# Kernel tuning notes

Hardware: AMD Instinct MI355X
Metric: run time of the kernel (lower is better)

The kernel has to match this reference:

```python
import jax, jax.numpy as jnp
import numpy as np

B, S, H, D, P = 16, 512, 12, 768, 256
TOP_RATE = 0.1
K = int(round(TOP_RATE * S))  # 51, matches round(self.top_rate * hidden_state.size(1))
LN_EPS = 1e-5


def setup_inputs() -> dict:
    key = jax.random.key(0)
    ks = jax.random.split(key, 6)
    return {
        "hidden_state": jax.random.normal(ks[0], (B, S, D), dtype=jnp.float32),
        "attention": jax.random.normal(ks[1], (B, H, S, S), dtype=jnp.float32),
        "length": S,  # uniform valid length (scalar int)
        # node_trans: Linear(D, P)
        "W_node": jax.random.normal(ks[2], (D, P), dtype=jnp.float32) * 0.02,
        "b_node": jnp.zeros((P,), dtype=jnp.float32),
        # node_eta parameter, initialized to 0 (self.node_eta.data.fill_(0))
        "node_eta": jnp.zeros((1,), dtype=jnp.float32),
        # fc: Linear(P, P)
        "W_fc": jax.random.normal(ks[3], (P, P), dtype=jnp.float32) * 0.02,
        "b_fc": jnp.zeros((P,), dtype=jnp.float32),
        # LayerNorm(P)
        "ln_gamma": jnp.ones((P,), dtype=jnp.float32),
        "ln_beta": jnp.zeros((P,), dtype=jnp.float32),
    }


def reference(hidden_state, attention, W_node, b_node, node_eta, W_fc, b_fc,
              ln_gamma, ln_beta, length):
    # average attention over heads: [B, S, S]
    avg_atten = attention.mean(axis=1)
    # per-target-node top-k neighbors
    vals, idx = jax.lax.top_k(avg_atten, K)  # [B, S, K]
    # edge mask replicating softmax(where(v>0, v, -1e9)) followed by nonzero():
    # entries at -1e9 underflow to exactly 0 in fp32 softmax iff the row has a
    # positive value; otherwise the softmax is uniform and all edges survive.
    keep = vals > 0.0
    row_has_pos = keep.any(axis=-1, keepdims=True)
    keep = jnp.where(row_has_pos, keep, True)            # [B, S, K] (>=1 True per row)
    keepf = keep.astype(hidden_state.dtype)[..., None]   # [B, S, K, 1]

    # node_trans on all nodes: [B, S, P]
    h = hidden_state @ W_node + b_node

    # gather source-node features h[b, idx[b, t, j], :] -> [B, S, K, P]
    gathered = jax.vmap(lambda hb, ib: hb[ib])(h, idx)

    # reduce='mean': edge weight w=1, mailbox mean over kept incoming edges
    h_agg = (gathered * keepf).sum(axis=2) / keepf.sum(axis=2)

    eta = node_eta[0]
    new_h = eta * h + (1.0 - eta) * h_agg                # [B, S, P]

    # dgl.mean_nodes: mean over the `length` nodes of each sub-graph (=S here)
    out = new_h.mean(axis=1)                             # [B, P]

    # fc(dropout(tanh(out))) with dropout in eval mode (identity)
    out = jnp.tanh(out) @ W_fc + b_fc

    # LayerNorm
    mu = out.mean(axis=-1, keepdims=True)
    var = ((out - mu) ** 2).mean(axis=-1, keepdims=True)
    out = (out - mu) / jnp.sqrt(var + LN_EPS) * ln_gamma + ln_beta
    return out
```

## Files before the change

### kernel.cpp

```cpp
#include <hip/hip_runtime.h>
#include <math.h>

#define B_ 16
#define S_ 512
#define H_ 12
#define D_ 768
#define P_ 256
#define K_ 51
#define CH_ 16
#define NCHUNK_ (S_/CH_)

__device__ __forceinline__ unsigned okey(float f) {
  unsigned u = __float_as_uint(f);
  return (u & 0x80000000u) ? ~u : (u | 0x80000000u);
}

__global__ __launch_bounds__(256, 8) void k1_topk_mask(
    const float* __restrict__ attn, unsigned long long* __restrict__ maskbuf,
    float* __restrict__ invbuf) {
  const int tid = threadIdx.x;
  const int wv = tid >> 6;
  const int lane = tid & 63;
  const int bt = blockIdx.x * 4 + wv;
  const int b = bt >> 9;
  const int t = bt & (S_ - 1);

  const float* base = attn + (((size_t)b * H_) * S_ + t) * S_;
  float a[8] = {0.f, 0.f, 0.f, 0.f, 0.f, 0.f, 0.f, 0.f};
  #pragma unroll
  for (int h = 0; h < H_; ++h) {
    const float* r = base + (size_t)h * (S_ * S_);
    const float4 u = *(const float4*)(r + 4 * lane);
    const float4 v = *(const float4*)(r + 256 + 4 * lane);
    a[0] += u.x; a[1] += u.y; a[2] += u.z; a[3] += u.w;
    a[4] += v.x; a[5] += v.y; a[6] += v.z; a[7] += v.w;
  }
  unsigned k[8];
  #pragma unroll
  for (int i = 0; i < 8; ++i) {
    a[i] *= (1.0f / (float)H_);
    k[i] = okey(a[i]);
  }

  int p = 0;
  #pragma unroll
  for (int i = 0; i < 8; ++i) p += __popcll(__ballot(a[i] > 0.f));

  bool sel[8];
  float invcnt;
  if (p >= 1 && p < K_) {
    #pragma unroll
    for (int i = 0; i < 8; ++i) sel[i] = (a[i] > 0.f);
    invcnt = 1.0f / (float)p;
  } else {
    unsigned prefix = 0;
    unsigned rem = K_;
    #pragma unroll
    for (int bpos = 31; bpos >= 0; --bpos) {
      const unsigned cand = prefix | (1u << bpos);
      const unsigned ch = cand >> bpos;
      unsigned cnt = 0;
      #pragma unroll
      for (int i = 0; i < 8; ++i)
        cnt += (unsigned)__popcll(__ballot((k[i] >> bpos) == ch));
      const bool ge = (cnt >= rem);
      prefix = ge ? cand : prefix;
      rem = ge ? rem : (rem - cnt);
    }
    const unsigned T = prefix;
    unsigned long long mm[8];
    #pragma unroll
    for (int i = 0; i < 8; ++i) mm[i] = __ballot(k[i] == T);
    const unsigned long long lt = ((unsigned long long)1 << lane) - 1ull;
    int fh = 0;
    #pragma unroll
    for (int i = 0; i < 4; ++i) fh += __popcll(mm[i]);
    #pragma unroll
    for (int i = 0; i < 8; ++i) {
      sel[i] = (k[i] > T);
      if (k[i] == T) {
        int r = 0;
        if (i < 4) {
          #pragma unroll
          for (int i2 = 0; i2 < 4; ++i2) r += __popcll(mm[i2] & lt);
          for (int i2 = 0; i2 < i; ++i2) r += (int)((mm[i2] >> lane) & 1ull);
        } else {
          r = fh;
          #pragma unroll
          for (int i2 = 4; i2 < 8; ++i2) r += __popcll(mm[i2] & lt);
          for (int i2 = 4; i2 < i; ++i2) r += (int)((mm[i2] >> lane) & 1ull);
        }
        if (r < (int)rem) sel[i] = true;
      }
    }
    invcnt = 1.0f / (float)K_;
  }

  unsigned long long m[8];
  #pragma unroll
  for (int i = 0; i < 8; ++i) m[i] = __ballot(sel[i]);
  if (lane == 0) {
    ulonglong2* mp = (ulonglong2*)(maskbuf + (size_t)bt * 8);
    mp[0] = ulonglong2{m[0], m[1]};
    mp[1] = ulonglong2{m[2], m[3]};
    mp[2] = ulonglong2{m[4], m[5]};
    mp[3] = ulonglong2{m[6], m[7]};
    invbuf[bt] = invcnt;
  }
}

__global__ __launch_bounds__(192) void k2_colsum_wsum(
    const unsigned long long* __restrict__ maskbuf,
    const float* __restrict__ invbuf, const float* __restrict__ node_eta,
    const float* __restrict__ hidden, float* __restrict__ x_part) {
  const int chunk = blockIdx.x;
  const int b = blockIdx.y;
  const int tid = threadIdx.x;
  __shared__ unsigned long long ld[S_ * 4];
  __shared__ float inv[S_];
  __shared__ float part[16][8];
  __shared__ float cs[CH_];

  const int wi0 = (chunk < 16) ? 0 : 4;
  for (int i = tid; i < S_ * 4; i += 192) {
    const int t = i >> 2, j = i & 3;
    ld[i] = maskbuf[(((size_t)b << 9) + t) * 8 + wi0 + j];
  }
  for (int i = tid; i < S_; i += 192) inv[i] = invbuf[(b << 9) + i];
  __syncthreads();

  if (tid < 128) {
    const int c = tid >> 3, g = tid & 7;
    const int s = chunk * CH_ + c;
    const int j = s & 3;
    const unsigned long long bm = 1ull << ((s & 255) >> 2);
    float w = 0.f;
    #pragma unroll 8
    for (int i = 0; i < 64; ++i) {
      const int t = i * 8 + g;
      if (ld[t * 4 + j] & bm) w += inv[t];
    }
    part[c][g] = w;
  }
  __syncthreads();
  if (tid < CH_) {
    float w = 0.f;
    #pragma unroll
    for (int g = 0; g < 8; ++g) w += part[tid][g];
    const float eta = node_eta[0];
    cs[tid] = (eta + (1.0f - eta) * w) * (1.0f / (float)S_);
  }
  __syncthreads();

  const float* hb = hidden + ((size_t)b * S_ + (size_t)chunk * CH_) * D_ + 4 * tid;
  float4 acc = make_float4(0.f, 0.f, 0.f, 0.f);
  #pragma unroll
  for (int s = 0; s < CH_; ++s) {
    const float4 v = *(const float4*)(hb + (size_t)s * D_);
    const float c = cs[s];
    acc.x += c * v.x; acc.y += c * v.y; acc.z += c * v.z; acc.w += c * v.w;
  }
  *(float4*)(x_part + ((size_t)chunk * B_ + b) * D_ + 4 * tid) = acc;
}

__global__ __launch_bounds__(256) void k3_tail(
    const float* __restrict__ x_part, const float* __restrict__ W_node,
    const float* __restrict__ b_node, const float* __restrict__ W_fc,
    const float* __restrict__ b_fc, const float* __restrict__ gamma,
    const float* __restrict__ beta, float* __restrict__ out) {
  const int b = blockIdx.x;
  const int tid = threadIdx.x;
  __shared__ float xs[D_];
  __shared__ float ts[P_];
  __shared__ float red[4];

  #pragma unroll
  for (int d = tid; d < D_; d += 256) {
    float s = 0.f;
    #pragma unroll 8
    for (int c = 0; c < NCHUNK_; ++c)
      s += x_part[((size_t)c * B_ + b) * D_ + d];
    xs[d] = s;
  }
  __syncthreads();

  float acc = 0.f;
  #pragma unroll 8
  for (int d = 0; d < D_; ++d) acc += xs[d] * W_node[(size_t)d * P_ + tid];
  ts[tid] = tanhf(acc + b_node[tid]);
  __syncthreads();

  float o = 0.f;
  #pragma unroll 8
  for (int q = 0; q < P_; ++q) o += ts[q] * W_fc[(size_t)q * P_ + tid];
  o += b_fc[tid];

  float s = o;
  #pragma unroll
  for (int off = 32; off > 0; off >>= 1) s += __shfl_down(s, off, 64);
  const int wave = tid >> 6, lane = tid & 63;
  if (lane == 0) red[wave] = s;
  __syncthreads();
  const float mu = (red[0] + red[1] + red[2] + red[3]) * (1.0f / (float)P_);
  __syncthreads();
  const float dv = o - mu;
  float s2 = dv * dv;
  #pragma unroll
  for (int off = 32; off > 0; off >>= 1) s2 += __shfl_down(s2, off, 64);
  if (lane == 0) red[wave] = s2;
  __syncthreads();
  const float var = (red[0] + red[1] + red[2] + red[3]) * (1.0f / (float)P_);
  const float inv = 1.0f / sqrtf(var + 1e-5f);
  out[b * P_ + tid] = dv * inv * gamma[tid] + beta[tid];
}

extern "C" void kernel_launch(void* const* d_in, const int* in_sizes, int n_in,
                              void* d_out, int out_size, void* d_ws, size_t ws_size,
                              hipStream_t stream) {
  (void)in_sizes; (void)n_in; (void)out_size; (void)ws_size;
  const float* hidden   = (const float*)d_in[0];
  const float* attn     = (const float*)d_in[1];
  const float* W_node   = (const float*)d_in[3];
  const float* b_node   = (const float*)d_in[4];
  const float* node_eta = (const float*)d_in[5];
  const float* W_fc     = (const float*)d_in[6];
  const float* b_fc     = (const float*)d_in[7];
  const float* gamma    = (const float*)d_in[8];
  const float* beta     = (const float*)d_in[9];
  float* out = (float*)d_out;

  unsigned long long* maskbuf = (unsigned long long*)d_ws;
  float* invbuf = (float*)(maskbuf + (size_t)B_ * S_ * 8);
  float* x_part = invbuf + B_ * S_;

  k1_topk_mask<<<(B_ * S_) / 4, 256, 0, stream>>>(attn, maskbuf, invbuf);
  k2_colsum_wsum<<<dim3(NCHUNK_, B_), 192, 0, stream>>>(maskbuf, invbuf,
                                                        node_eta, hidden, x_part);
  k3_tail<<<B_, 256, 0, stream>>>(x_part, W_node, b_node, W_fc, b_fc,
                                  gamma, beta, out);
}
```

Measured before the change: 383.2 us.

## Split serial tail kernel into parallel reduce, matvec, fc and layernorm kernels

The single 16-block tail kernel, which did the chunk reduction, both matvecs and the layernorm serially per batch, is split into four kernels. Each matvec is now spread over many blocks, with threads splitting the reduction dimension and combining partial sums in shared memory. This is meant to fix the low parallelism of the tail, which ran only 16 blocks on a large GPU. In exchange it adds three extra kernel launches and global round trips through new workspace buffers.

```diff
diff --git a/kernel.cpp b/kernel.cpp
--- a/kernel.cpp
+++ b/kernel.cpp
@@ -163,38 +163,90 @@
   *(float4*)(x_part + ((size_t)chunk * B_ + b) * D_ + 4 * tid) = acc;
 }
 
-__global__ __launch_bounds__(256) void k3_tail(
-    const float* __restrict__ x_part, const float* __restrict__ W_node,
-    const float* __restrict__ b_node, const float* __restrict__ W_fc,
-    const float* __restrict__ b_fc, const float* __restrict__ gamma,
+__global__ __launch_bounds__(256) void k2b_reduce(
+    const float* __restrict__ x_part, float* __restrict__ x) {
+  const int d = blockIdx.x * 256 + threadIdx.x;
+  const int b = blockIdx.y;
+  float s = 0.f;
+  #pragma unroll 8
+  for (int c = 0; c < NCHUNK_; ++c)
+    s += x_part[((size_t)c * B_ + b) * D_ + d];
+  x[b * D_ + d] = s;
+}
+
+__global__ __launch_bounds__(256) void k3a_tanh_matvec(
+    const float* __restrict__ x, const float* __restrict__ W_node,
+    const float* __restrict__ b_node, float* __restrict__ tbuf) {
+  const int j = blockIdx.x;
+  const int b = blockIdx.y;
+  const int tid = threadIdx.x;
+  const int pp = tid & 15;
+  const int g = tid >> 4;
+  __shared__ float xs[D_];
+  __shared__ float part[16][32];
+  for (int d = tid; d < D_; d += 256) xs[d] = x[b * D_ + d];
+  __syncthreads();
+  const float* Wp = W_node + 32 * j + 2 * pp;
+  float2 acc = make_float2(0.f, 0.f);
+  const int d0 = 48 * g;
+  #pragma unroll 8
+  for (int dd = 0; dd < 48; ++dd) {
+    const int d = d0 + dd;
+    const float2 wv = *(const float2*)(Wp + (size_t)d * P_);
+    const float xv = xs[d];
+    acc.x += xv * wv.x; acc.y += xv * wv.y;
+  }
+  *(float2*)&part[g][2 * pp] = acc;
+  __syncthreads();
+  if (tid < 32) {
+    float s = 0.f;
+    #pragma unroll
+    for (int gg = 0; gg < 16; ++gg) s += part[gg][tid];
+    const int pcol = 32 * j + tid;
+    tbuf[b * P_ + pcol] = tanhf(s + b_node[pcol]);
+  }
+}
+
+__global__ __launch_bounds__(256) void k3b_fc(
+    const float* __restrict__ tbuf, const float* __restrict__ W_fc,
+    const float* __restrict__ b_fc, float* __restrict__ obuf) {
+  const int j = blockIdx.x;
+  const int b = blockIdx.y;
+  const int tid = threadIdx.x;
+  const int pp = tid & 31;
+  const int g = tid >> 5;
+  __shared__ float ts[P_];
+  __shared__ float part[8][64];
+  ts[tid] = tbuf[b * P_ + tid];
+  __syncthreads();
+  const float* Wp = W_fc + 64 * j + 2 * pp;
+  float2 acc = make_float2(0.f, 0.f);
+  const int q0 = 32 * g;
+  #pragma unroll 8
+  for (int qq = 0; qq < 32; ++qq) {
+    const int q = q0 + qq;
+    const float2 wv = *(const float2*)(Wp + (size_t)q * P_);
+    const float tv = ts[q];
+    acc.x += tv * wv.x; acc.y += tv * wv.y;
+  }
+  *(float2*)&part[g][2 * pp] = acc;
+  __syncthreads();
+  if (tid < 64) {
+    float s = 0.f;
+    #pragma unroll
+    for (int gg = 0; gg < 8; ++gg) s += part[gg][tid];
+    const int pcol = 64 * j + tid;
+    obuf[b * P_ + pcol] = s + b_fc[pcol];
+  }
+}
+
+__global__ __launch_bounds__(256) void k3c_layernorm(
+    const float* __restrict__ obuf, const float* __restrict__ gamma,
     const float* __restrict__ beta, float* __restrict__ out) {
   const int b = blockIdx.x;
   const int tid = threadIdx.x;
-  __shared__ float xs[D_];
-  __shared__ float ts[P_];
   __shared__ float red[4];
-
-  #pragma unroll
-  for (int d = tid; d < D_; d += 256) {
-    float s = 0.f;
-    #pragma unroll 8
-    for (int c = 0; c < NCHUNK_; ++c)
-      s += x_part[((size_t)c * B_ + b) * D_ + d];
-    xs[d] = s;
-  }
-  __syncthreads();
-
-  float acc = 0.f;
-  #pragma unroll 8
-  for (int d = 0; d < D_; ++d) acc += xs[d] * W_node[(size_t)d * P_ + tid];
-  ts[tid] = tanhf(acc + b_node[tid]);
-  __syncthreads();
-
-  float o = 0.f;
-  #pragma unroll 8
-  for (int q = 0; q < P_; ++q) o += ts[q] * W_fc[(size_t)q * P_ + tid];
-  o += b_fc[tid];
-
+  const float o = obuf[b * P_ + tid];
   float s = o;
   #pragma unroll
   for (int off = 32; off > 0; off >>= 1) s += __shfl_down(s, off, 64);
@@ -232,10 +284,15 @@
   unsigned long long* maskbuf = (unsigned long long*)d_ws;
   float* invbuf = (float*)(maskbuf + (size_t)B_ * S_ * 8);
   float* x_part = invbuf + B_ * S_;
+  float* x      = x_part + (size_t)NCHUNK_ * B_ * D_;
+  float* tbuf   = x + B_ * D_;
+  float* obuf   = tbuf + B_ * P_;
 
   k1_topk_mask<<<(B_ * S_) / 4, 256, 0, stream>>>(attn, maskbuf, invbuf);
   k2_colsum_wsum<<<dim3(NCHUNK_, B_), 192, 0, stream>>>(maskbuf, invbuf,
                                                         node_eta, hidden, x_part);
-  k3_tail<<<B_, 256, 0, stream>>>(x_part, W_node, b_node, W_fc, b_fc,
-                                  gamma, beta, out);
-}
+  k2b_reduce<<<dim3(3, B_), 256, 0, stream>>>(x_part, x);
+  k3a_tanh_matvec<<<dim3(8, B_), 256, 0, stream>>>(x, W_node, b_node, tbuf);
+  k3b_fc<<<dim3(4, B_), 256, 0, stream>>>(tbuf, W_fc, b_fc, obuf);
+  k3c_layernorm<<<B_, 256, 0, stream>>>(obuf, gamma, beta, out);
+}
```

After: 331.2 us. 13.6% less time.
